# Kernel tuning notes

Measured on AMD Instinct MI355X. Metric: run time of the kernel, lower is better.

## Reference

```python
import jax, jax.numpy as jnp
import numpy as np

B, S, D_IN, D_MID, D_OUT, V = 32, 512, 768, 128, 4, 100000
N = B * S  # static upper bound on number of unique (vocab_id, batch_id) pairs


def setup_inputs() -> dict:
    key = jax.random.key(0)
    k1, k2, k3, k4 = jax.random.split(key, 4)
    vocab_ids = jax.random.randint(k1, (B, S), 0, V)
    embeddings = jax.random.normal(k2, (B, S, D_IN), jnp.float32)
    # nn.Linear default init (kaiming-uniform-ish); exact distribution is irrelevant for correctness
    lin_bound = 1.0 / np.sqrt(D_IN)
    W1 = jax.random.uniform(k3, (D_IN, D_MID), jnp.float32, -lin_bound, lin_bound)
    b1 = jnp.zeros((D_MID,), jnp.float32)
    # kaiming_uniform_(a=sqrt(5)) on (V, D_MID, D_OUT): fan_in = D_MID*D_OUT, bound = 1/sqrt(fan_in)
    enc_bound = 1.0 / np.sqrt(D_MID * D_OUT)
    encoder_weights = jax.random.uniform(k4, (V, D_MID, D_OUT), jnp.float32, -enc_bound, enc_bound)
    return {"vocab_ids": vocab_ids, "embeddings": embeddings, "W1": W1, "b1": b1,
            "encoder_weights": encoder_weights}


def reference(vocab_ids, embeddings, W1, b1, encoder_weights):
    # Composite key = vocab_id * B + batch_id -> same lexicographic (vocab, batch) order
    # as torch.unique(dim=0) on stacked (vocab_id, batch_id) pairs.
    batch_ids = jnp.arange(B, dtype=vocab_ids.dtype)[:, None]            # (B,1)
    keys = (vocab_ids * B + batch_ids).reshape(-1)                        # (N,)
    # Static-size unique for jit; padded slots (fill) receive zero-sum embeddings.
    uniq_keys, inv = jnp.unique(keys, size=N, fill_value=0, return_inverse=True)
    flat_emb = embeddings.reshape(N, D_IN)
    summed = jax.ops.segment_sum(flat_emb, inv.reshape(-1), num_segments=N)  # (N, D_IN)
    h = jnp.tanh(summed @ W1 + b1)                                        # (N, D_MID)
    uniq_vocab = uniq_keys // B
    uniq_batch = uniq_keys % B
    Wtok = encoder_weights[uniq_vocab]                                    # (N, D_MID, D_OUT) gather
    encoded = jax.nn.sigmoid(jnp.einsum('bi,bio->bo', h, Wtok))           # (N, D_OUT)
    ids = jnp.stack([uniq_vocab, uniq_batch], axis=1)                     # (N, 2)
    return ids, encoded
```

## Files before the change

kernel.cpp:

```cpp
#include <hip/hip_runtime.h>
#include <hip/hip_bf16.h>

#define NELEM 16384
#define DIN 768
#define DMID 128
#define DOUT 4

typedef __attribute__((ext_vector_type(8))) short short8;
typedef __attribute__((ext_vector_type(4))) float f32x4;

__device__ __forceinline__ unsigned f2bf(float f) {
    unsigned u = __float_as_uint(f);
    return (u + 0x7FFFu + ((u >> 16) & 1u)) >> 16;
}
__device__ __forceinline__ unsigned wscan_inc(unsigned x, int lane) {
    unsigned inc = x;
#pragma unroll
    for (int off = 1; off < 64; off <<= 1) {
        unsigned y = __shfl_up(inc, off);
        if (lane >= off) inc += y;
    }
    return inc;
}
__device__ __forceinline__ unsigned popc4(uint4 x) {
    return (unsigned)(__popc(x.x) + __popc(x.y) + __popc(x.z) + __popc(x.w));
}

#define FAST5_WS 983168

__global__ __launch_bounds__(256) void prep_kernel(
    const int* __restrict__ vocab_ids, const float* __restrict__ W1,
    unsigned* __restrict__ Gb, unsigned short* __restrict__ WtG,
    unsigned* __restrict__ RBT, unsigned long long* __restrict__ stage,
    unsigned* __restrict__ LCnt) {
    __shared__ unsigned lbm[4096];
    __shared__ unsigned voc[512];
    __shared__ unsigned short gel[512];
    __shared__ unsigned gcnt[512];
    __shared__ unsigned gstart[512];
    __shared__ unsigned part[256];
    __shared__ unsigned wsumL[4];

    const int t = threadIdx.x;
    const int b = blockIdx.x;
    const int lane = t & 63;
    const int wv = t >> 6;

#pragma unroll
    for (int i = 0; i < 12; ++i) {
        int j = b * 3072 + i * 256 + t;
        int k = j >> 7, c = j & 127;
        WtG[c * DIN + k] = (unsigned short)f2bf(W1[j]);
    }

#pragma unroll
    for (int i = 0; i < 16; ++i) lbm[t + 256 * i] = 0;
    gcnt[t] = 0; gcnt[t + 256] = 0;
#pragma unroll
    for (int q = 0; q < 2; ++q) {
        int s = q * 256 + t;
        voc[s] = (unsigned)vocab_ids[b * 512 + s];
    }
    __syncthreads();
#pragma unroll
    for (int q = 0; q < 2; ++q) {
        unsigned v = voc[q * 256 + t];
        atomicOr(&lbm[v >> 5], 1u << (v & 31u));
    }
    __syncthreads();
#pragma unroll
    for (int i = 0; i < 16; ++i) {
        int w = i * 256 + t;
        RBT[w * 32 + b] = lbm[w];
    }
    {
        unsigned sum = 0;
#pragma unroll
        for (int j = 0; j < 16; ++j) sum += (unsigned)__popc(lbm[t * 16 + j]);
        unsigned inc = wscan_inc(sum, lane);
        if (lane == 63) wsumL[wv] = inc;
        __syncthreads();
        unsigned woff = 0;
        for (int i = 0; i < wv; ++i) woff += wsumL[i];
        part[t] = woff + inc - sum;
        if (t == 255) LCnt[b] = woff + inc;
        __syncthreads();
    }
#pragma unroll
    for (int q = 0; q < 2; ++q) {
        int s = q * 256 + t;
        unsigned v = voc[s];
        unsigned lw = v >> 5, c = lw >> 4;
        unsigned g = part[c];
        for (unsigned j = c * 16; j < lw; ++j) g += (unsigned)__popc(lbm[j]);
        g += (unsigned)__popc(lbm[lw] & ((1u << (v & 31u)) - 1u));
        gel[s] = (unsigned short)g;
        atomicAdd(&gcnt[g], 1u);
    }
    __syncthreads();
    {
        unsigned a = gcnt[2 * t], b2 = gcnt[2 * t + 1];
        unsigned pair = a + b2;
        unsigned inc = wscan_inc(pair, lane);
        if (lane == 63) wsumL[wv] = inc;
        __syncthreads();
        unsigned woff = 0;
        for (int i = 0; i < wv; ++i) woff += wsumL[i];
        unsigned excl = woff + inc - pair;
        gstart[2 * t] = excl;
        gstart[2 * t + 1] = excl + a;
    }
    __syncthreads();
#pragma unroll
    for (int q = 0; q < 2; ++q) {
        int s = q * 256 + t;
        unsigned g = gel[s];
        unsigned v = voc[s];
        unsigned m = 0;
        if (gcnt[g] > 1) {
            for (int j = 0; j < s; ++j) if (voc[j] == v) ++m;
        }
        Gb[b * 512 + gstart[g] + m] = (v << 9) | (unsigned)s;
        if (m == 0) {
            unsigned sdval = ((unsigned)b << 19) | (gstart[g] << 10) | gcnt[g];
            stage[b * 512 + g] = ((unsigned long long)v << 32) | sdval;
        }
    }
}

__global__ __launch_bounds__(256) void rank_kernel(
    const unsigned* __restrict__ RBT,
    const unsigned long long* __restrict__ stage,
    const unsigned* __restrict__ LCnt,
    unsigned* __restrict__ SD, float* __restrict__ out_ids) {
    __shared__ unsigned pre1[4096];
    __shared__ unsigned wsumL[4];
    __shared__ unsigned Ush;

    const int t = threadIdx.x;
    const int b = blockIdx.x;
    const int lane = t & 63;
    const int wv = t >> 6;
    const uint4* rb4 = (const uint4*)RBT;

    {
        unsigned loc[16];
        unsigned run = 0;
#pragma unroll
        for (int i = 0; i < 16; ++i) {
            loc[i] = run;
            const uint4* p = rb4 + (t * 16 + i) * 8;
            unsigned s = 0;
#pragma unroll
            for (int q = 0; q < 8; ++q) s += popc4(p[q]);
            run += s;
        }
        unsigned inc = wscan_inc(run, lane);
        if (lane == 63) wsumL[wv] = inc;
        __syncthreads();
        unsigned woff = 0;
        for (int i = 0; i < wv; ++i) woff += wsumL[i];
        unsigned excl = woff + inc - run;
#pragma unroll
        for (int i = 0; i < 16; ++i) pre1[t * 16 + i] = excl + loc[i];
        if (t == 255) Ush = woff + inc;
        __syncthreads();
    }
    const unsigned U = Ush;

    const unsigned cnt = LCnt[b];
    for (unsigned l = t; l < cnt; l += 256) {
        unsigned long long sv = stage[b * 512 + l];
        unsigned v = (unsigned)(sv >> 32);
        unsigned sdval = (unsigned)sv;
        unsigned w = v >> 5, bit = v & 31u;
        unsigned maskLT = (1u << bit) - 1u;
        unsigned rank = pre1[w];
        const unsigned* col = RBT + w * 32;
#pragma unroll
        for (int bb = 0; bb < 32; ++bb) {
            unsigned word = col[bb];
            rank += (unsigned)__popc(word & maskLT);
            if (bb < b) rank += (word >> bit) & 1u;
        }
        SD[rank] = sdval;
        out_ids[2 * rank + 0] = (float)v;
        out_ids[2 * rank + 1] = (float)b;
    }
    for (int u = (int)U + b * 256 + t; u < NELEM; u += 32 * 256) {
        SD[u] = 0u;
        out_ids[2 * u + 0] = 0.0f;
        out_ids[2 * u + 1] = 0.0f;
    }
}

#define FBM 16
__global__ __launch_bounds__(256) void fused_kernel(
    const unsigned* __restrict__ Gb,
    const unsigned* __restrict__ SD,
    const unsigned short* __restrict__ WtG,
    const float* __restrict__ emb,
    const float* __restrict__ b1,
    const float* __restrict__ enc,
    float* __restrict__ out_enc) {
    __shared__ char smem[20736];

    const int t = threadIdx.x;
    const int u0 = blockIdx.x * FBM;
    const int l = t & 63;
    const int w = t >> 6;

    const int ar = t >> 4;
    const int ak4 = t & 15;
    const unsigned sdw = SD[u0 + ar];
    const int lenA = (int)(sdw & 1023u);
    const unsigned embBase = (sdw >> 19) << 9;
    const unsigned gb0 = embBase + ((sdw >> 10) & 511u);

    f32x4 acc0 = {0.f, 0.f, 0.f, 0.f};
    f32x4 acc1 = {0.f, 0.f, 0.f, 0.f};

    for (int kk = 0; kk < DIN; kk += 64) {
        __syncthreads();
        {
            float s0 = 0.f, s1 = 0.f, s2 = 0.f, s3 = 0.f;
            const float* base = emb + (size_t)(kk + ak4 * 4);
            for (int p = 0; p < lenA; ++p) {
                unsigned idx = embBase + (Gb[gb0 + p] & 511u);
                const float4 e4 = *(const float4*)(base + (size_t)idx * DIN);
                s0 += e4.x; s1 += e4.y; s2 += e4.z; s3 += e4.w;
            }
            uint2 packed;
            packed.x = f2bf(s0) | (f2bf(s1) << 16);
            packed.y = f2bf(s2) | (f2bf(s3) << 16);
            *(uint2*)(smem + ar * 144 + ak4 * 8) = packed;
        }
        {
#pragma unroll
            for (int i = 0; i < 4; ++i) {
                int q = t + i * 256;
                int c = q >> 3;
                int uo = q & 7;
                uint4 dv = *(const uint4*)(WtG + (size_t)c * DIN + kk + uo * 8);
                *(uint4*)(smem + 2304 + c * 144 + uo * 16) = dv;
            }
        }
        __syncthreads();
        {
            const int arow = l & 15;
            const int ull = l >> 4;
#pragma unroll
            for (int kf = 0; kf < 2; ++kf) {
                short8 aF = *(const short8*)(smem + arow * 144 + kf * 64 + ull * 16);
                short8 bF0 = *(const short8*)(smem + 2304 + (w * 32 + arow) * 144 + kf * 64 + ull * 16);
                short8 bF1 = *(const short8*)(smem + 2304 + (w * 32 + 16 + arow) * 144 + kf * 64 + ull * 16);
                acc0 = __builtin_amdgcn_mfma_f32_16x16x32_bf16(aF, bF0, acc0, 0, 0, 0);
                acc1 = __builtin_amdgcn_mfma_f32_16x16x32_bf16(aF, bF1, acc1, 0, 0, 0);
            }
        }
    }
    __syncthreads();
    {
        float* Hs = (float*)smem;
        const int col0 = w * 32 + (l & 15);
        const int rbase = (l >> 4) * 4;
#pragma unroll
        for (int reg = 0; reg < 4; ++reg) {
            Hs[(rbase + reg) * 132 + col0] = tanhf(acc0[reg] + b1[col0]);
            Hs[(rbase + reg) * 132 + col0 + 16] = tanhf(acc1[reg] + b1[col0 + 16]);
        }
    }
    __syncthreads();
    {
        const float* Hs = (const float*)smem;
        const int r = t >> 4;
        const int g = t & 15;
        const int u = u0 + r;
        const unsigned sdw2 = SD[u];
        unsigned vocab = 0;
        if (sdw2 & 1023u)
            vocab = Gb[((sdw2 >> 19) << 9) + ((sdw2 >> 10) & 511u)] >> 9;
        const float4* wrow = (const float4*)(enc + (size_t)vocab * (DMID * DOUT));
        float ax = 0.f, ay = 0.f, az = 0.f, aw = 0.f;
#pragma unroll
        for (int jj = 0; jj < 8; ++jj) {
            int j = jj * 16 + g;
            float4 w4 = wrow[j];
            float hv = Hs[r * 132 + j];
            ax += hv * w4.x; ay += hv * w4.y; az += hv * w4.z; aw += hv * w4.w;
        }
#pragma unroll
        for (int off = 1; off < 16; off <<= 1) {
            ax += __shfl_xor(ax, off);
            ay += __shfl_xor(ay, off);
            az += __shfl_xor(az, off);
            aw += __shfl_xor(aw, off);
        }
        if (g == 0) {
            float4 o;
            o.x = 1.f / (1.f + expf(-ax));
            o.y = 1.f / (1.f + expf(-ay));
            o.z = 1.f / (1.f + expf(-az));
            o.w = 1.f / (1.f + expf(-aw));
            *(float4*)(out_enc + (size_t)u * 4) = o;
        }
    }
}

#define SORT_SMEM (65536 + 65536 + 4096 + 64)

__global__ __launch_bounds__(1024) void sort_transpose_kernel(
    const int* __restrict__ vocab_ids,
    const float* __restrict__ W1,
    unsigned int* __restrict__ G,
    unsigned short* __restrict__ RS,
    unsigned short* __restrict__ WtG,
    float* __restrict__ out_ids) {
    const int t = threadIdx.x;
    if (blockIdx.x != 0) {
        int idx = (blockIdx.x - 1) * 1024 + t;
        if (idx < DMID * DIN) {
            int c = idx / DIN;
            int k = idx - c * DIN;
            WtG[idx] = (unsigned short)f2bf(W1[k * DMID + c]);
        }
        return;
    }
    extern __shared__ char smem[];
    unsigned* Gs     = (unsigned*)smem;
    unsigned* histDM = (unsigned*)(smem + 65536);
    unsigned* sums   = (unsigned*)(smem + 131072);
    unsigned* totalU = (unsigned*)(smem + 135168);
    for (int e = t; e < NELEM; e += 1024)
        Gs[e] = ((unsigned)vocab_ids[e] << 14) | (unsigned)e;
    __syncthreads();
    for (int pass = 0; pass < 6; ++pass) {
        const int shift = 9 + pass * 4;
        unsigned v[16];
#pragma unroll
        for (int i = 0; i < 16; ++i) v[i] = Gs[t * 16 + i];
#pragma unroll
        for (int d = 0; d < 16; ++d) histDM[d * 1024 + t] = 0;
#pragma unroll
        for (int i = 0; i < 16; ++i) histDM[((v[i] >> shift) & 15u) * 1024 + t] += 1;
        __syncthreads();
        unsigned lex[16]; unsigned run = 0;
#pragma unroll
        for (int i = 0; i < 16; ++i) { unsigned x = histDM[t * 16 + i]; lex[i] = run; run += x; }
        sums[t] = run;
        __syncthreads();
        if (t < 64) {
            unsigned s[16]; unsigned tot = 0;
#pragma unroll
            for (int i = 0; i < 16; ++i) { unsigned x = sums[t * 16 + i]; s[i] = tot; tot += x; }
            unsigned incv = tot;
#pragma unroll
            for (int off = 1; off < 64; off <<= 1) {
                unsigned y = __shfl_up(incv, off);
                if (t >= off) incv += y;
            }
            unsigned excl = incv - tot;
#pragma unroll
            for (int i = 0; i < 16; ++i) sums[t * 16 + i] = excl + s[i];
        }
        __syncthreads();
#pragma unroll
        for (int i = 0; i < 16; ++i) histDM[t * 16 + i] = sums[t] + lex[i];
        __syncthreads();
        unsigned mycnt[16];
#pragma unroll
        for (int d = 0; d < 16; ++d) mycnt[d] = histDM[d * 1024 + t];
#pragma unroll
        for (int i = 0; i < 16; ++i) {
            unsigned d = (v[i] >> shift) & 15u;
            Gs[mycnt[d]++] = v[i];
        }
        __syncthreads();
    }
    unsigned v[16];
#pragma unroll
    for (int i = 0; i < 16; ++i) v[i] = Gs[t * 16 + i];
    unsigned pk = (t == 0) ? 0xFFFFFFFFu : (Gs[t * 16 - 1] >> 9);
    unsigned fm = 0;
#pragma unroll
    for (int i = 0; i < 16; ++i) {
        unsigned key = v[i] >> 9;
        if (key != pk) fm |= (1u << i);
        pk = key;
    }
    sums[t] = (unsigned)__popc(fm);
    __syncthreads();
    if (t < 64) {
        unsigned s[16]; unsigned tot = 0;
#pragma unroll
        for (int i = 0; i < 16; ++i) { unsigned x = sums[t * 16 + i]; s[i] = tot; tot += x; }
        unsigned incv = tot;
#pragma unroll
        for (int off = 1; off < 64; off <<= 1) {
            unsigned y = __shfl_up(incv, off);
            if (t >= off) incv += y;
        }
        unsigned excl = incv - tot;
#pragma unroll
        for (int i = 0; i < 16; ++i) sums[t * 16 + i] = excl + s[i];
        if (t == 63) *totalU = incv;
    }
    __syncthreads();
    unsigned r = sums[t];
#pragma unroll
    for (int i = 0; i < 16; ++i) {
        if (fm & (1u << i)) {
            RS[r] = (unsigned short)(t * 16 + i);
            out_ids[2 * r + 0] = (float)(v[i] >> 14);
            out_ids[2 * r + 1] = (float)((v[i] >> 9) & 31u);
            ++r;
        }
    }
    const unsigned U = *totalU;
    for (int u = t; u < NELEM; u += 1024) {
        if ((unsigned)u >= U) {
            RS[u] = (unsigned short)NELEM;
            out_ids[2 * u + 0] = 0.0f;
            out_ids[2 * u + 1] = 0.0f;
        }
        G[u] = Gs[u];
    }
    if (t == 0) RS[NELEM] = (unsigned short)NELEM;
}

__global__ __launch_bounds__(256) void fused_kernel_rs(
    const unsigned* __restrict__ G,
    const unsigned short* __restrict__ RS,
    const unsigned short* __restrict__ WtG,
    const float* __restrict__ emb,
    const float* __restrict__ b1,
    const float* __restrict__ enc,
    float* __restrict__ out_enc) {
    __shared__ char smem[20736];
    const int t = threadIdx.x;
    const int u0 = blockIdx.x * FBM;
    const int l = t & 63;
    const int w = t >> 6;
    const int ar = t >> 4;
    const int ak4 = t & 15;
    const int rs_a = (int)RS[u0 + ar];
    const int re_a = (int)RS[u0 + ar + 1];
    f32x4 acc0 = {0.f, 0.f, 0.f, 0.f};
    f32x4 acc1 = {0.f, 0.f, 0.f, 0.f};
    for (int kk = 0; kk < DIN; kk += 64) {
        __syncthreads();
        {
            float s0 = 0.f, s1 = 0.f, s2 = 0.f, s3 = 0.f;
            const float* base = emb + (size_t)(kk + ak4 * 4);
            for (int p = rs_a; p < re_a; ++p) {
                unsigned idx = G[p] & 16383u;
                const float4 e4 = *(const float4*)(base + (size_t)idx * DIN);
                s0 += e4.x; s1 += e4.y; s2 += e4.z; s3 += e4.w;
            }
            uint2 packed;
            packed.x = f2bf(s0) | (f2bf(s1) << 16);
            packed.y = f2bf(s2) | (f2bf(s3) << 16);
            *(uint2*)(smem + ar * 144 + ak4 * 8) = packed;
        }
        {
#pragma unroll
            for (int i = 0; i < 4; ++i) {
                int q = t + i * 256;
                int c = q >> 3;
                int uo = q & 7;
                uint4 dv = *(const uint4*)(WtG + (size_t)c * DIN + kk + uo * 8);
                *(uint4*)(smem + 2304 + c * 144 + uo * 16) = dv;
            }
        }
        __syncthreads();
        {
            const int arow = l & 15;
            const int ull = l >> 4;
#pragma unroll
            for (int kf = 0; kf < 2; ++kf) {
                short8 aF = *(const short8*)(smem + arow * 144 + kf * 64 + ull * 16);
                short8 bF0 = *(const short8*)(smem + 2304 + (w * 32 + arow) * 144 + kf * 64 + ull * 16);
                short8 bF1 = *(const short8*)(smem + 2304 + (w * 32 + 16 + arow) * 144 + kf * 64 + ull * 16);
                acc0 = __builtin_amdgcn_mfma_f32_16x16x32_bf16(aF, bF0, acc0, 0, 0, 0);
                acc1 = __builtin_amdgcn_mfma_f32_16x16x32_bf16(aF, bF1, acc1, 0, 0, 0);
            }
        }
    }
    __syncthreads();
    {
        float* Hs = (float*)smem;
        const int col0 = w * 32 + (l & 15);
        const int rbase = (l >> 4) * 4;
#pragma unroll
        for (int reg = 0; reg < 4; ++reg) {
            Hs[(rbase + reg) * 132 + col0] = tanhf(acc0[reg] + b1[col0]);
            Hs[(rbase + reg) * 132 + col0 + 16] = tanhf(acc1[reg] + b1[col0 + 16]);
        }
    }
    __syncthreads();
    {
        const float* Hs = (const float*)smem;
        const int r = t >> 4;
        const int g = t & 15;
        const int u = u0 + r;
        const int rs = (int)RS[u];
        const int re = (int)RS[u + 1];
        unsigned vocab = (rs < re) ? (G[rs] >> 14) : 0u;
        const float4* wrow = (const float4*)(enc + (size_t)vocab * (DMID * DOUT));
        float ax = 0.f, ay = 0.f, az = 0.f, aw = 0.f;
#pragma unroll
        for (int jj = 0; jj < 8; ++jj) {
            int j = jj * 16 + g;
            float4 w4 = wrow[j];
            float hv = Hs[r * 132 + j];
            ax += hv * w4.x; ay += hv * w4.y; az += hv * w4.z; aw += hv * w4.w;
        }
#pragma unroll
        for (int off = 1; off < 16; off <<= 1) {
            ax += __shfl_xor(ax, off);
            ay += __shfl_xor(ay, off);
            az += __shfl_xor(az, off);
            aw += __shfl_xor(aw, off);
        }
        if (g == 0) {
            float4 o;
            o.x = 1.f / (1.f + expf(-ax));
            o.y = 1.f / (1.f + expf(-ay));
            o.z = 1.f / (1.f + expf(-az));
            o.w = 1.f / (1.f + expf(-aw));
            *(float4*)(out_enc + (size_t)u * 4) = o;
        }
    }
}

extern "C" void kernel_launch(void* const* d_in, const int* in_sizes, int n_in,
                              void* d_out, int out_size, void* d_ws, size_t ws_size,
                              hipStream_t stream) {
    const int*   vocab_ids = (const int*)d_in[0];
    const float* emb       = (const float*)d_in[1];
    const float* W1        = (const float*)d_in[2];
    const float* b1        = (const float*)d_in[3];
    const float* enc       = (const float*)d_in[4];
    float* out = (float*)d_out;
    float* out_ids = out;
    float* out_enc = out + NELEM * 2;
    char* ws = (char*)d_ws;

    if (ws_size >= FAST5_WS) {
        unsigned*           Gb    = (unsigned*)(ws + 0);
        unsigned*           SD    = (unsigned*)(ws + 65536);
        unsigned short*     WtG   = (unsigned short*)(ws + 131072);
        unsigned long long* stage = (unsigned long long*)(ws + 327680);
        unsigned*           LCnt  = (unsigned*)(ws + 458752);
        unsigned*           RBT   = (unsigned*)(ws + 458880);

        prep_kernel<<<32, 256, 0, stream>>>(vocab_ids, W1, Gb, WtG, RBT, stage, LCnt);
        rank_kernel<<<32, 256, 0, stream>>>(RBT, stage, LCnt, SD, out_ids);
        fused_kernel<<<NELEM / FBM, 256, 0, stream>>>(Gb, SD, WtG, emb, b1, enc, out_enc);
    } else {
        unsigned int*   G   = (unsigned int*)(ws);
        unsigned short* RS  = (unsigned short*)(ws + 65536);
        unsigned short* WtG = (unsigned short*)(ws + 98432);

        hipFuncSetAttribute((const void*)sort_transpose_kernel,
                            hipFuncAttributeMaxDynamicSharedMemorySize, SORT_SMEM);
        sort_transpose_kernel<<<1 + 96, 1024, SORT_SMEM, stream>>>(
            vocab_ids, W1, G, RS, WtG, out_ids);
        fused_kernel_rs<<<NELEM / FBM, 256, 0, stream>>>(G, RS, WtG, emb, b1, enc, out_enc);
    }
}
```

Measured before the change: 70.07 us.

## Store per-batch bitmaps row-major and split W1 transpose into extra blocks

The per-batch vocab bitmaps now go out row-major with coalesced uint4 stores instead of the transposed [word][batch] layout. The rank kernel's prefix popcount is reorganised to stream over batches with coalesced uint4 loads. The W1-to-bf16 transpose moves out of the 32 bitmap blocks into 96 extra blocks, each writing packed pairs, so it runs in parallel with the bitmap work. The per-element rank lookup now reads a strided column across the 32 rows, which is less local than before.

```diff
diff --git a/kernel.cpp b/kernel.cpp
--- a/kernel.cpp
+++ b/kernel.cpp
@@ -22,17 +22,28 @@
     }
     return inc;
 }
-__device__ __forceinline__ unsigned popc4(uint4 x) {
-    return (unsigned)(__popc(x.x) + __popc(x.y) + __popc(x.z) + __popc(x.w));
-}
-
-#define FAST5_WS 983168
+
+#define FAST6_WS 983168
 
 __global__ __launch_bounds__(256) void prep_kernel(
     const int* __restrict__ vocab_ids, const float* __restrict__ W1,
     unsigned* __restrict__ Gb, unsigned short* __restrict__ WtG,
-    unsigned* __restrict__ RBT, unsigned long long* __restrict__ stage,
+    unsigned* __restrict__ RB, unsigned long long* __restrict__ stage,
     unsigned* __restrict__ LCnt) {
+    const int t = threadIdx.x;
+    const int blk = blockIdx.x;
+
+    if (blk >= 32) {
+        int o = (blk - 32) * 1024 + t * 4;
+        int c = o / DIN;
+        int k = o - c * DIN;
+        unsigned p0 = f2bf(W1[(k + 0) * DMID + c]) | (f2bf(W1[(k + 1) * DMID + c]) << 16);
+        unsigned p1 = f2bf(W1[(k + 2) * DMID + c]) | (f2bf(W1[(k + 3) * DMID + c]) << 16);
+        uint2 pk2; pk2.x = p0; pk2.y = p1;
+        *(uint2*)(WtG + (size_t)c * DIN + k) = pk2;
+        return;
+    }
+
     __shared__ unsigned lbm[4096];
     __shared__ unsigned voc[512];
     __shared__ unsigned short gel[512];
@@ -41,17 +52,9 @@
     __shared__ unsigned part[256];
     __shared__ unsigned wsumL[4];
 
-    const int t = threadIdx.x;
-    const int b = blockIdx.x;
+    const int b = blk;
     const int lane = t & 63;
     const int wv = t >> 6;
-
-#pragma unroll
-    for (int i = 0; i < 12; ++i) {
-        int j = b * 3072 + i * 256 + t;
-        int k = j >> 7, c = j & 127;
-        WtG[c * DIN + k] = (unsigned short)f2bf(W1[j]);
-    }
 
 #pragma unroll
     for (int i = 0; i < 16; ++i) lbm[t + 256 * i] = 0;
@@ -69,9 +72,12 @@
     }
     __syncthreads();
 #pragma unroll
-    for (int i = 0; i < 16; ++i) {
-        int w = i * 256 + t;
-        RBT[w * 32 + b] = lbm[w];
+    for (int i = 0; i < 4; ++i) {
+        int w4 = i * 256 + t;
+        uint4 x;
+        x.x = lbm[w4 * 4 + 0]; x.y = lbm[w4 * 4 + 1];
+        x.z = lbm[w4 * 4 + 2]; x.w = lbm[w4 * 4 + 3];
+        *(uint4*)(RB + (size_t)b * 4096 + w4 * 4) = x;
     }
     {
         unsigned sum = 0;
@@ -129,7 +135,7 @@
 }
 
 __global__ __launch_bounds__(256) void rank_kernel(
-    const unsigned* __restrict__ RBT,
+    const unsigned* __restrict__ RB,
     const unsigned long long* __restrict__ stage,
     const unsigned* __restrict__ LCnt,
     unsigned* __restrict__ SD, float* __restrict__ out_ids) {
@@ -141,20 +147,28 @@
     const int b = blockIdx.x;
     const int lane = t & 63;
     const int wv = t >> 6;
-    const uint4* rb4 = (const uint4*)RBT;
-
-    {
+    const uint4* rb4 = (const uint4*)RB;
+
+    {
+        unsigned cs[16];
+#pragma unroll
+        for (int i = 0; i < 16; ++i) cs[i] = 0;
+#pragma unroll 4
+        for (int b2 = 0; b2 < 32; ++b2) {
+            const uint4* rp = rb4 + b2 * 1024 + t * 4;
+#pragma unroll
+            for (int q = 0; q < 4; ++q) {
+                uint4 x = rp[q];
+                cs[q * 4 + 0] += (unsigned)__popc(x.x);
+                cs[q * 4 + 1] += (unsigned)__popc(x.y);
+                cs[q * 4 + 2] += (unsigned)__popc(x.z);
+                cs[q * 4 + 3] += (unsigned)__popc(x.w);
+            }
+        }
         unsigned loc[16];
         unsigned run = 0;
 #pragma unroll
-        for (int i = 0; i < 16; ++i) {
-            loc[i] = run;
-            const uint4* p = rb4 + (t * 16 + i) * 8;
-            unsigned s = 0;
-#pragma unroll
-            for (int q = 0; q < 8; ++q) s += popc4(p[q]);
-            run += s;
-        }
+        for (int i = 0; i < 16; ++i) { loc[i] = run; run += cs[i]; }
         unsigned inc = wscan_inc(run, lane);
         if (lane == 63) wsumL[wv] = inc;
         __syncthreads();
@@ -176,12 +190,11 @@
         unsigned w = v >> 5, bit = v & 31u;
         unsigned maskLT = (1u << bit) - 1u;
         unsigned rank = pre1[w];
-        const unsigned* col = RBT + w * 32;
-#pragma unroll
-        for (int bb = 0; bb < 32; ++bb) {
-            unsigned word = col[bb];
+#pragma unroll 8
+        for (int b2 = 0; b2 < 32; ++b2) {
+            unsigned word = RB[b2 * 4096 + w];
             rank += (unsigned)__popc(word & maskLT);
-            if (bb < b) rank += (word >> bit) & 1u;
+            if (b2 < b) rank += (word >> bit) & 1u;
         }
         SD[rank] = sdval;
         out_ids[2 * rank + 0] = (float)v;
@@ -546,16 +559,16 @@
     float* out_enc = out + NELEM * 2;
     char* ws = (char*)d_ws;
 
-    if (ws_size >= FAST5_WS) {
+    if (ws_size >= FAST6_WS) {
         unsigned*           Gb    = (unsigned*)(ws + 0);
         unsigned*           SD    = (unsigned*)(ws + 65536);
         unsigned short*     WtG   = (unsigned short*)(ws + 131072);
         unsigned long long* stage = (unsigned long long*)(ws + 327680);
         unsigned*           LCnt  = (unsigned*)(ws + 458752);
-        unsigned*           RBT   = (unsigned*)(ws + 458880);
-
-        prep_kernel<<<32, 256, 0, stream>>>(vocab_ids, W1, Gb, WtG, RBT, stage, LCnt);
-        rank_kernel<<<32, 256, 0, stream>>>(RBT, stage, LCnt, SD, out_ids);
+        unsigned*           RB    = (unsigned*)(ws + 458880);
+
+        prep_kernel<<<128, 256, 0, stream>>>(vocab_ids, W1, Gb, WtG, RB, stage, LCnt);
+        rank_kernel<<<32, 256, 0, stream>>>(RB, stage, LCnt, SD, out_ids);
         fused_kernel<<<NELEM / FBM, 256, 0, stream>>>(Gb, SD, WtG, emb, b1, enc, out_enc);
     } else {
         unsigned int*   G   = (unsigned int*)(ws);
```

Result: faster. 60.08 us (-14.3%).
